# Performance work log

Measured on AMD Instinct MI355X. Metric: run time of the kernel, lower is better.

## Reference

```python
import jax, jax.numpy as jnp
import numpy as np

N, E = 50000, 800000
D_IN, HID, HEADS, D_OUT = 128, 32, 4, 40
NEG_SLOPE = 0.2
BN_EPS = 1e-5


def gat_conv(x, src, dst, W, a_src, a_dst, b, heads, ch):
    """PyG-style GATConv (eval mode, self-loops already appended to src/dst)."""
    n = x.shape[0]
    h = (x @ W).reshape(n, heads, ch)                      # [N,H,C]
    al_src = jnp.einsum('nhc,hc->nh', h, a_src)            # [N,H]
    al_dst = jnp.einsum('nhc,hc->nh', h, a_dst)
    e = jax.nn.leaky_relu(al_src[src] + al_dst[dst], NEG_SLOPE)  # [Etot,H]
    # segment softmax over incoming edges of each dst node
    e_max = jax.ops.segment_max(e, dst, num_segments=n)
    e = jnp.exp(e - e_max[dst])
    denom = jax.ops.segment_sum(e, dst, num_segments=n)
    alpha = e / (denom[dst] + 1e-16)                        # [Etot,H]
    msg = h[src] * alpha[:, :, None]                        # [Etot,H,C]
    out = jax.ops.segment_sum(msg, dst, num_segments=n)     # [N,H,C]
    return out.reshape(n, heads * ch) + b


def bn_eval(x, g, b, m, v):
    return (x - m) * jax.lax.rsqrt(v + BN_EPS) * g + b


def setup_inputs() -> dict:
    key = jax.random.key(0)
    ks = jax.random.split(key, 24)
    p = lambda k, s: jax.random.normal(k, s, jnp.float32) * 0.1
    inp = {
        'x': jax.random.normal(ks[0], (N, D_IN), jnp.float32),
        'edge_index': jax.random.randint(ks[1], (2, E), 0, N),
        'W1': p(ks[2], (D_IN, HEADS * HID)),
        'a_src1': p(ks[3], (HEADS, HID)), 'a_dst1': p(ks[4], (HEADS, HID)),
        'b1': jnp.zeros((HEADS * HID,), jnp.float32),
        'W2': p(ks[5], (HEADS * HID, HEADS * HID)),
        'a_src2': p(ks[6], (HEADS, HID)), 'a_dst2': p(ks[7], (HEADS, HID)),
        'b2': jnp.zeros((HEADS * HID,), jnp.float32),
        'W3': p(ks[8], (HEADS * HID, D_OUT)),
        'a_src3': p(ks[9], (1, D_OUT)), 'a_dst3': p(ks[10], (1, D_OUT)),
        'b3': jnp.zeros((D_OUT,), jnp.float32),
        'bn1_g': jnp.ones((HEADS * HID,), jnp.float32),
        'bn1_b': jnp.zeros((HEADS * HID,), jnp.float32),
        'bn1_m': p(ks[11], (HEADS * HID,)),
        'bn1_v': jax.random.uniform(ks[12], (HEADS * HID,), jnp.float32) + 0.5,
        'bn2_g': jnp.ones((HEADS * HID,), jnp.float32),
        'bn2_b': jnp.zeros((HEADS * HID,), jnp.float32),
        'bn2_m': p(ks[13], (HEADS * HID,)),
        'bn2_v': jax.random.uniform(ks[14], (HEADS * HID,), jnp.float32) + 0.5,
    }
    return inp


def reference(x, edge_index, W1, a_src1, a_dst1, b1, W2, a_src2, a_dst2, b2,
              W3, a_src3, a_dst3, b3, bn1_g, bn1_b, bn1_m, bn1_v,
              bn2_g, bn2_b, bn2_m, bn2_v):
    n = x.shape[0]
    loop = jnp.arange(n, dtype=edge_index.dtype)
    src = jnp.concatenate([edge_index[0], loop])   # add self loops (PyG default)
    dst = jnp.concatenate([edge_index[1], loop])

    h = gat_conv(x, src, dst, W1, a_src1, a_dst1, b1, HEADS, HID)
    h = jax.nn.relu(h)
    h = bn_eval(h, bn1_g, bn1_b, bn1_m, bn1_v)      # dropout = identity (eval)

    h = gat_conv(h, src, dst, W2, a_src2, a_dst2, b2, HEADS, HID)
    h = jax.nn.relu(h)
    h = bn_eval(h, bn2_g, bn2_b, bn2_m, bn2_v)

    h = gat_conv(h, src, dst, W3, a_src3, a_dst3, b3, 1, D_OUT)
    return jax.nn.log_softmax(h, axis=1)
```

## Files before the change

### kernel.cpp

```cpp
#include <hip/hip_runtime.h>
#include <hip/hip_bf16.h>
#include <math.h>

using bf16 = __hip_bfloat16;
using frag8 = __attribute__((ext_vector_type(8))) short;
using f32x4 = __attribute__((ext_vector_type(4))) float;

#define LEAKY 0.2f
#define BN_EPS 1e-5f
#define NEGBIG -1e30f

__device__ __forceinline__ float lrelu(float z){ return z > 0.f ? z : LEAKY * z; }
__device__ __forceinline__ float bflo(unsigned u){ return __uint_as_float(u << 16); }
__device__ __forceinline__ float bfhi(unsigned u){ return __uint_as_float(u & 0xffff0000u); }
__device__ __forceinline__ unsigned pk(float a, float b){
  unsigned ua = __float_as_uint(a), ub = __float_as_uint(b);
  ua += 0x7fffu + ((ua >> 16) & 1u);
  ub += 0x7fffu + ((ub >> 16) & 1u);
  return (ua >> 16) | (ub & 0xffff0000u);
}
__device__ __forceinline__ float ldf(const void* p, size_t i, int isbf){
  if (isbf) return (float)((const bf16*)p)[i];
  return ((const float*)p)[i];
}

union U4F8 { uint4 u; frag8 f; };

__device__ __forceinline__ frag8 load_a_pairs(const unsigned* __restrict__ X2, int node, int k0){
  U4F8 v; v.u = *((const uint4*)(X2 + (size_t)node*64 + (k0 >> 1))); return v.f;
}
__device__ __forceinline__ frag8 load_a_f32(const float* __restrict__ X, int node, int k0){
  float4 q0 = *((const float4*)(X + (size_t)node*128 + k0));
  float4 q1 = *((const float4*)(X + (size_t)node*128 + k0 + 4));
  U4F8 v; v.u = make_uint4(pk(q0.x,q0.y), pk(q0.z,q0.w), pk(q1.x,q1.y), pk(q1.z,q1.w));
  return v.f;
}

__global__ void init_detect(int* head, const unsigned short* __restrict__ w1bits,
                            int* flag, int n){
  int g = blockIdx.x*256 + threadIdx.x;
  if (g < n) head[g] = -1;
  if (blockIdx.x == 0){
    __shared__ int cntr;
    if (threadIdx.x == 0) cntr = 0;
    __syncthreads();
    unsigned u = w1bits[threadIdx.x * 2];
    int e = (u >> 7) & 0xff;
    atomicAdd(&cntr, (e >= 64 && e <= 140) ? 1 : 0);
    __syncthreads();
    if (threadIdx.x == 0) *flag = (cntr >= 160) ? 1 : 0;
  }
}

__global__ void chain_build(const int* __restrict__ dst, int* head, int* next,
                            int e, int n){
  int g = blockIdx.x*256 + threadIdx.x;
  if (g < e){
    int d = dst[g];
    next[g] = ((unsigned)d < (unsigned)n) ? atomicExch(&head[d], g) : -1;
  }
}

__global__ void chain_count(const int* __restrict__ head, const int* __restrict__ next,
                            int* cnt, int* total, int n){
  int g = blockIdx.x*256 + threadIdx.x;
  if (g == 0) *total = 0;
  if (g >= n) return;
  int c = 0;
  for (int e = head[g]; e != -1; e = next[e]) ++c;
  cnt[g] = c;
}

__global__ void csr_scan(const int* __restrict__ cnt, int* start, int* total, int n){
  __shared__ int s[256];
  __shared__ int base_s;
  int t = threadIdx.x;
  int g = blockIdx.x*256 + t;
  int v = (g < n) ? cnt[g] : 0;
  s[t] = v;
  __syncthreads();
  for (int off = 1; off < 256; off <<= 1){
    int x = (t >= off) ? s[t-off] : 0;
    __syncthreads();
    s[t] += x;
    __syncthreads();
  }
  if (t == 255) base_s = atomicAdd(total, s[255]);
  __syncthreads();
  if (g < n) start[g] = base_s + s[t] - v;
}

__global__ void chain_fill(const int* __restrict__ head, const int* __restrict__ next,
                           const int* __restrict__ src, const int* __restrict__ start,
                           int* col, int n){
  int g = blockIdx.x*256 + threadIdx.x;
  if (g >= n) return;
  int p = start[g];
  for (int e = head[g]; e != -1; e = next[e])
    col[p++] = src[e];
}

__global__ __launch_bounds__(256) void gemm_al_mfma(
    const void* __restrict__ X, int xkind,
    const void* __restrict__ W, const void* __restrict__ Wsrc, const void* __restrict__ Wdst,
    const int* __restrict__ flagp,
    unsigned* __restrict__ H2, float* __restrict__ AL, float* __restrict__ AD,
    int n, int ntiles)
{
  __shared__ unsigned short WT[128*136];
  const int isbf = *flagp;
  const int t = threadIdx.x;
  if (isbf){
    const unsigned short* W16 = (const unsigned short*)W;
    for (int idx = t; idx < 16384; idx += 256){
      int k = idx >> 7, nn = idx & 127;
      WT[nn*136 + k] = W16[idx];
    }
  } else {
    const float* Wf = (const float*)W;
    for (int idx = t; idx < 16384; idx += 256){
      int k = idx >> 7, nn = idx & 127;
      WT[nn*136 + k] = (unsigned short)(pk(Wf[idx], 0.f) & 0xffffu);
    }
  }
  __syncthreads();
  const int w = t >> 6;
  const int lane = t & 63;
  const int m = lane & 15, quad = lane >> 4;

  frag8 bf[4][2];
  #pragma unroll
  for (int s = 0; s < 4; ++s)
    #pragma unroll
    for (int ct = 0; ct < 2; ++ct){
      int colc = w*32 + ct*16 + m;
      int k0 = s*32 + quad*8;
      U4F8 v; v.u = *((const uint4*)&WT[colc*136 + k0]);
      bf[s][ct] = v.f;
    }
  float avv[2], dvv[2];
  #pragma unroll
  for (int ct = 0; ct < 2; ++ct){
    int colc = w*32 + ct*16 + m;
    avv[ct] = ldf(Wsrc, colc, isbf);
    dvv[ct] = ldf(Wdst, colc, isbf);
  }
  const bool pairs = (xkind == 1) || isbf;

  for (int tile = blockIdx.x; tile < ntiles; tile += gridDim.x){
    const int mb = tile*16;
    int nodeA = mb + m; if (nodeA >= n) nodeA = n - 1;
    frag8 af[4];
    #pragma unroll
    for (int s = 0; s < 4; ++s){
      int k0 = s*32 + quad*8;
      af[s] = pairs ? load_a_pairs((const unsigned*)X, nodeA, k0)
                    : load_a_f32((const float*)X, nodeA, k0);
    }
    f32x4 acc0 = {0.f,0.f,0.f,0.f}, acc1 = {0.f,0.f,0.f,0.f};
    #pragma unroll
    for (int s = 0; s < 4; ++s){
      acc0 = __builtin_amdgcn_mfma_f32_16x16x32_bf16(af[s], bf[s][0], acc0, 0,0,0);
      acc1 = __builtin_amdgcn_mfma_f32_16x16x32_bf16(af[s], bf[s][1], acc1, 0,0,0);
    }
    #pragma unroll
    for (int r = 0; r < 4; ++r){
      int g = mb + quad*4 + r;
      float v0 = acc0[r], v1 = acc1[r];
      unsigned u0 = pk(v0, __shfl_xor(v0, 1));
      unsigned u1 = pk(v1, __shfl_xor(v1, 1));
      bool ok = g < n;
      if (((lane & 1) == 0) && ok){
        H2[(size_t)g*64 + w*16 + (m >> 1)]     = u0;
        H2[(size_t)g*64 + w*16 + 8 + (m >> 1)] = u1;
      }
      float s1 = v0*avv[0] + v1*avv[1];
      float s2 = v0*dvv[0] + v1*dvv[1];
      s1 += __shfl_xor(s1,1); s1 += __shfl_xor(s1,2); s1 += __shfl_xor(s1,4); s1 += __shfl_xor(s1,8);
      s2 += __shfl_xor(s2,1); s2 += __shfl_xor(s2,2); s2 += __shfl_xor(s2,4); s2 += __shfl_xor(s2,8);
      if (m == 0 && ok){ AL[g*4 + w] = s1; AD[g*4 + w] = s2; }
    }
  }
}

__global__ __launch_bounds__(256) void gemm3_mfma(
    const unsigned* __restrict__ X2, const void* __restrict__ W,
    const void* __restrict__ Wsrc, const void* __restrict__ Wdst,
    const int* __restrict__ flagp,
    unsigned* __restrict__ H3, float* __restrict__ AL, float* __restrict__ AD,
    int n, int ntiles)
{
  __shared__ unsigned short WT[48*136];
  const int isbf = *flagp;
  const int t = threadIdx.x;
  for (int idx = t; idx < 128*64; idx += 256){
    int c = idx & 63, k = idx >> 6;
    if (c < 48){
      unsigned short v = 0;
      if (c < 40){
        if (isbf) v = ((const unsigned short*)W)[k*40 + c];
        else      v = (unsigned short)(pk(((const float*)W)[k*40 + c], 0.f) & 0xffffu);
      }
      WT[c*136 + k] = v;
    }
  }
  __syncthreads();
  const int w = t >> 6;
  const int lane = t & 63;
  const int m = lane & 15, quad = lane >> 4;

  frag8 bf[4][3];
  float avv[3], dvv[3];
  #pragma unroll
  for (int ct = 0; ct < 3; ++ct){
    int colc = ct*16 + m;
    #pragma unroll
    for (int s = 0; s < 4; ++s){
      int k0 = s*32 + quad*8;
      U4F8 v; v.u = *((const uint4*)&WT[colc*136 + k0]);
      bf[s][ct] = v.f;
    }
    avv[ct] = (colc < 40) ? ldf(Wsrc, colc, isbf) : 0.f;
    dvv[ct] = (colc < 40) ? ldf(Wdst, colc, isbf) : 0.f;
  }

  for (int tg = blockIdx.x; tg*4 < ntiles; tg += gridDim.x){
    const int tile = tg*4 + w;
    if (tile >= ntiles) continue;
    const int mb = tile*16;
    int nodeA = mb + m; if (nodeA >= n) nodeA = n - 1;
    frag8 af[4];
    #pragma unroll
    for (int s = 0; s < 4; ++s)
      af[s] = load_a_pairs(X2, nodeA, s*32 + quad*8);
    f32x4 acc[3];
    #pragma unroll
    for (int ct = 0; ct < 3; ++ct) acc[ct] = (f32x4){0.f,0.f,0.f,0.f};
    #pragma unroll
    for (int s = 0; s < 4; ++s){
      acc[0] = __builtin_amdgcn_mfma_f32_16x16x32_bf16(af[s], bf[s][0], acc[0], 0,0,0);
      acc[1] = __builtin_amdgcn_mfma_f32_16x16x32_bf16(af[s], bf[s][1], acc[1], 0,0,0);
      acc[2] = __builtin_amdgcn_mfma_f32_16x16x32_bf16(af[s], bf[s][2], acc[2], 0,0,0);
    }
    #pragma unroll
    for (int r = 0; r < 4; ++r){
      int g = mb + quad*4 + r;
      bool ok = g < n;
      float ps = 0.f, pd = 0.f;
      #pragma unroll
      for (int ct = 0; ct < 3; ++ct){
        float v = acc[ct][r];
        ps += v*avv[ct]; pd += v*dvv[ct];
        unsigned u = pk(v, __shfl_xor(v, 1));
        bool stok = ((lane & 1) == 0) && ok && (ct < 2 || m < 8);
        if (stok) H3[(size_t)g*20 + ct*8 + (m >> 1)] = u;
      }
      ps += __shfl_xor(ps,1); ps += __shfl_xor(ps,2); ps += __shfl_xor(ps,4); ps += __shfl_xor(ps,8);
      pd += __shfl_xor(pd,1); pd += __shfl_xor(pd,2); pd += __shfl_xor(pd,4); pd += __shfl_xor(pd,8);
      if (m == 0 && ok){ AL[g] = ps; AD[g] = pd; }
    }
  }
}

__global__ __launch_bounds__(256) void agg4(
    const unsigned* __restrict__ H2,
    const float* __restrict__ ALf, const float* __restrict__ ADf,
    const int* __restrict__ cnt, const int* __restrict__ start, const int* __restrict__ col,
    const void* __restrict__ bias, const void* __restrict__ bng, const void* __restrict__ bnb,
    const void* __restrict__ bnm,  const void* __restrict__ bnv,
    const int* __restrict__ flagp,
    unsigned* __restrict__ Hout, int n)
{
  const int isbf = *flagp;
  const int wave = threadIdx.x >> 6;
  const int lane = threadIdx.x & 63;
  const int node = blockIdx.x*4 + wave;
  if (node >= n) return;
  const int head = lane >> 4;
  const float ad = ADf[node*4 + head];
  const int base = start[node], deg = cnt[node];

  float accL, accH, l;
  {
    float e = __expf(lrelu(ALf[node*4 + head] + ad));
    unsigned h = H2[(size_t)node*64 + lane];
    l = e; accL = e * bflo(h); accH = e * bfhi(h);
  }

  int i = 0;
  for (; i + 8 <= deg; i += 8){
    int sv[8]; float av[8]; unsigned hv[8];
    #pragma unroll
    for (int u = 0; u < 8; ++u){
      int s = col[base + i + u];
      sv[u] = ((unsigned)s < (unsigned)n) ? s : 0;
    }
    #pragma unroll
    for (int u = 0; u < 8; ++u) av[u] = ALf[sv[u]*4 + head];
    #pragma unroll
    for (int u = 0; u < 8; ++u) hv[u] = H2[(size_t)sv[u]*64 + lane];
    #pragma unroll
    for (int u = 0; u < 8; ++u){
      float e = __expf(lrelu(av[u] + ad));
      l    += e;
      accL += e * bflo(hv[u]);
      accH += e * bfhi(hv[u]);
    }
  }
  for (; i < deg; ++i){
    int s = col[base + i];
    if ((unsigned)s >= (unsigned)n) s = 0;
    float a = ALf[s*4 + head];
    unsigned h = H2[(size_t)s*64 + lane];
    float e = __expf(lrelu(a + ad));
    l += e; accL += e * bflo(h); accH += e * bfhi(h);
  }

  const float rl = 1.f / l;
  const int c0 = 2*lane, c1 = c0 + 1;
  float v0 = fmaxf(accL*rl + ldf(bias,c0,isbf), 0.f);
  v0 = (v0 - ldf(bnm,c0,isbf)) * rsqrtf(ldf(bnv,c0,isbf) + BN_EPS) * ldf(bng,c0,isbf) + ldf(bnb,c0,isbf);
  float v1 = fmaxf(accH*rl + ldf(bias,c1,isbf), 0.f);
  v1 = (v1 - ldf(bnm,c1,isbf)) * rsqrtf(ldf(bnv,c1,isbf) + BN_EPS) * ldf(bng,c1,isbf) + ldf(bnb,c1,isbf);
  Hout[(size_t)node*64 + lane] = pk(v0, v1);
}

__global__ __launch_bounds__(256) void agg1(
    const unsigned* __restrict__ H3,
    const float* __restrict__ AL, const float* __restrict__ AD,
    const int* __restrict__ cnt, const int* __restrict__ start, const int* __restrict__ col,
    const void* __restrict__ b3, const int* __restrict__ flagp,
    void* __restrict__ out, int n)
{
  const int isbf = *flagp;
  const int wave = threadIdx.x >> 6;
  const int lane = threadIdx.x & 63;
  const int node = blockIdx.x*4 + wave;
  if (node >= n) return;
  const float ad = AD[node];
  const bool act = lane < 20;
  const int base = start[node], deg = cnt[node];

  float accL, accH, l;
  {
    float e = __expf(lrelu(AL[node] + ad));
    unsigned h = act ? H3[(size_t)node*20 + lane] : 0u;
    l = e; accL = e * bflo(h); accH = e * bfhi(h);
  }

  int i = 0;
  for (; i + 8 <= deg; i += 8){
    int sv[8]; float av[8]; unsigned hv[8];
    #pragma unroll
    for (int u = 0; u < 8; ++u){
      int s = col[base + i + u];
      sv[u] = ((unsigned)s < (unsigned)n) ? s : 0;
    }
    #pragma unroll
    for (int u = 0; u < 8; ++u) av[u] = AL[sv[u]];
    #pragma unroll
    for (int u = 0; u < 8; ++u) hv[u] = act ? H3[(size_t)sv[u]*20 + lane] : 0u;
    #pragma unroll
    for (int u = 0; u < 8; ++u){
      float e = __expf(lrelu(av[u] + ad));
      l    += e;
      accL += e * bflo(hv[u]);
      accH += e * bfhi(hv[u]);
    }
  }
  for (; i < deg; ++i){
    int s = col[base + i];
    if ((unsigned)s >= (unsigned)n) s = 0;
    float a = AL[s];
    unsigned h = act ? H3[(size_t)s*20 + lane] : 0u;
    float e = __expf(lrelu(a + ad));
    l += e; accL += e * bflo(h); accH += e * bfhi(h);
  }

  const float rl = 1.f / l;
  const int c0 = 2*lane;
  float z0 = act ? (accL*rl + ldf(b3, c0,     isbf)) : NEGBIG;
  float z1 = act ? (accH*rl + ldf(b3, c0 + 1, isbf)) : NEGBIG;
  float mx = fmaxf(z0, z1);
  #pragma unroll
  for (int off = 1; off < 64; off <<= 1) mx = fmaxf(mx, __shfl_xor(mx, off));
  float p = act ? (__expf(z0 - mx) + __expf(z1 - mx)) : 0.f;
  float sum = p;
  #pragma unroll
  for (int off = 1; off < 64; off <<= 1) sum += __shfl_xor(sum, off);
  if (act){
    float lg = __logf(sum);
    float r0 = z0 - mx - lg, r1 = z1 - mx - lg;
    if (isbf) ((unsigned*)out)[(size_t)node*20 + lane] = pk(r0, r1);
    else      ((float2*)out)[(size_t)node*20 + lane] = make_float2(r0, r1);
  }
}

extern "C" void kernel_launch(void* const* d_in, const int* in_sizes, int n_in,
                              void* d_out, int out_size, void* d_ws, size_t ws_size,
                              hipStream_t stream)
{
  (void)n_in; (void)out_size; (void)ws_size;
  const void* x    = d_in[0];
  const int*  ei   = (const int*)d_in[1];
  const void* W1   = d_in[2];
  const void* as1  = d_in[3];
  const void* ad1  = d_in[4];
  const void* b1   = d_in[5];
  const void* W2   = d_in[6];
  const void* as2  = d_in[7];
  const void* ad2  = d_in[8];
  const void* b2   = d_in[9];
  const void* W3   = d_in[10];
  const void* as3  = d_in[11];
  const void* ad3  = d_in[12];
  const void* b3   = d_in[13];
  const void* bn1g = d_in[14];
  const void* bn1b = d_in[15];
  const void* bn1m = d_in[16];
  const void* bn1v = d_in[17];
  const void* bn2g = d_in[18];
  const void* bn2b = d_in[19];
  const void* bn2m = d_in[20];
  const void* bn2v = d_in[21];

  const int N  = in_sizes[0] / 128;
  const int E  = in_sizes[1] / 2;
  const int ntiles = (N + 15) / 16;

  char* w = (char*)d_ws;
  size_t off = 0;
  auto alloc = [&](size_t bytes)->char*{
    char* p = w + off; off = (off + bytes + 255) & ~(size_t)255; return p;
  };
  unsigned* H2A = (unsigned*)alloc((size_t)N*64*4);
  unsigned* H2B = (unsigned*)alloc((size_t)N*64*4);
  unsigned* H3p = (unsigned*)alloc((size_t)N*20*4);
  float* AL   = (float*)alloc((size_t)N*4*4);
  float* AD   = (float*)alloc((size_t)N*4*4);
  int*   headp = (int*)alloc((size_t)N*4);
  int*   nextp = (int*)alloc((size_t)E*4);
  int*   cnt   = (int*)alloc((size_t)N*4);
  int*   start = (int*)alloc((size_t)N*4);
  int*   col   = (int*)alloc((size_t)E*4);
  int*   flag  = (int*)alloc(256);
  int*   total = (int*)alloc(256);

  const int* srcp = ei;
  const int* dstp = ei + E;

  const int nb256 = (N + 255)/256, eb256 = (E + 255)/256;
  const int bb = (N + 3)/4;
  int g1 = ntiles < 625 ? ntiles : 625;
  int g3 = (ntiles + 3)/4; if (g3 > 400) g3 = 400;

  init_detect<<<nb256,256,0,stream>>>(headp, (const unsigned short*)W1, flag, N);
  chain_build<<<eb256,256,0,stream>>>(dstp, headp, nextp, E, N);
  chain_count<<<nb256,256,0,stream>>>(headp, nextp, cnt, total, N);
  csr_scan  <<<nb256,256,0,stream>>>(cnt, start, total, N);
  chain_fill<<<nb256,256,0,stream>>>(headp, nextp, srcp, start, col, N);

  gemm_al_mfma<<<g1,256,0,stream>>>(x, 0, W1, as1, ad1, flag, H2A, AL, AD, N, ntiles);
  agg4<<<bb,256,0,stream>>>(H2A, AL, AD, cnt, start, col,
                            b1, bn1g, bn1b, bn1m, bn1v, flag, H2B, N);
  gemm_al_mfma<<<g1,256,0,stream>>>(H2B, 1, W2, as2, ad2, flag, H2A, AL, AD, N, ntiles);
  agg4<<<bb,256,0,stream>>>(H2A, AL, AD, cnt, start, col,
                            b2, bn2g, bn2b, bn2m, bn2v, flag, H2B, N);
  gemm3_mfma<<<g3,256,0,stream>>>(H2B, W3, as3, ad3, flag, H3p, AL, AD, N, ntiles);
  agg1<<<bb,256,0,stream>>>(H3p, AL, AD, cnt, start, col, b3, flag, d_out, N);
}
```

Measured before the change: 381.7 us.

## Precompute per-edge attention weights and split neighbor gather across half-waves

Adds per-edge weight kernels (wgt4/wgt1) that compute exp(leaky_relu(al_src+al_dst)) once per CSR edge, using a new rowid array written during CSR fill. The aggregation kernels then read these weights instead of gathering AL per neighbor and recomputing exp. agg4 now processes two neighbors at once, with each half-wave loading 8-byte feature chunks, and combines the halves with a cross-lane shuffle. The chain count is merged into the scan kernel to drop one launch. The cost is three extra kernel launches and a 16 B-per-edge weight array that must be written and read back.

```diff
diff --git a/kernel.cpp b/kernel.cpp
--- a/kernel.cpp
+++ b/kernel.cpp
@@ -37,9 +37,10 @@
 }
 
 __global__ void init_detect(int* head, const unsigned short* __restrict__ w1bits,
-                            int* flag, int n){
+                            int* flag, int* total, int n){
   int g = blockIdx.x*256 + threadIdx.x;
   if (g < n) head[g] = -1;
+  if (g == 0) *total = 0;
   if (blockIdx.x == 0){
     __shared__ int cntr;
     if (threadIdx.x == 0) cntr = 0;
@@ -61,22 +62,17 @@
   }
 }
 
-__global__ void chain_count(const int* __restrict__ head, const int* __restrict__ next,
-                            int* cnt, int* total, int n){
-  int g = blockIdx.x*256 + threadIdx.x;
-  if (g == 0) *total = 0;
-  if (g >= n) return;
-  int c = 0;
-  for (int e = head[g]; e != -1; e = next[e]) ++c;
-  cnt[g] = c;
-}
-
-__global__ void csr_scan(const int* __restrict__ cnt, int* start, int* total, int n){
+__global__ void csr_scan_walk(const int* __restrict__ head, const int* __restrict__ next,
+                              int* cnt, int* start, int* total, int n){
   __shared__ int s[256];
   __shared__ int base_s;
   int t = threadIdx.x;
   int g = blockIdx.x*256 + t;
-  int v = (g < n) ? cnt[g] : 0;
+  int v = 0;
+  if (g < n){
+    for (int e = head[g]; e != -1; e = next[e]) ++v;
+    cnt[g] = v;
+  }
   s[t] = v;
   __syncthreads();
   for (int off = 1; off < 256; off <<= 1){
@@ -92,12 +88,40 @@
 
 __global__ void chain_fill(const int* __restrict__ head, const int* __restrict__ next,
                            const int* __restrict__ src, const int* __restrict__ start,
-                           int* col, int n){
+                           int* col, int* rowid, int n){
   int g = blockIdx.x*256 + threadIdx.x;
   if (g >= n) return;
   int p = start[g];
-  for (int e = head[g]; e != -1; e = next[e])
-    col[p++] = src[e];
+  for (int e = head[g]; e != -1; e = next[e]){
+    int s = src[e];
+    if ((unsigned)s >= (unsigned)n) s = 0;
+    col[p] = s; rowid[p] = g; ++p;
+  }
+}
+
+__global__ void wgt4(const int* __restrict__ col, const int* __restrict__ rowid,
+                     const float4* __restrict__ AL4, const float4* __restrict__ AD4,
+                     float4* __restrict__ W4, int ecnt, int n){
+  int p = blockIdx.x*256 + threadIdx.x;
+  if (p >= ecnt) return;
+  int s = col[p];   if ((unsigned)s >= (unsigned)n) s = 0;
+  int d = rowid[p]; if ((unsigned)d >= (unsigned)n) d = 0;
+  float4 a = AL4[s], b = AD4[d];
+  float4 w;
+  w.x = __expf(lrelu(a.x + b.x));
+  w.y = __expf(lrelu(a.y + b.y));
+  w.z = __expf(lrelu(a.z + b.z));
+  w.w = __expf(lrelu(a.w + b.w));
+  W4[p] = w;
+}
+__global__ void wgt1(const int* __restrict__ col, const int* __restrict__ rowid,
+                     const float* __restrict__ AL, const float* __restrict__ AD,
+                     float* __restrict__ W1, int ecnt, int n){
+  int p = blockIdx.x*256 + threadIdx.x;
+  if (p >= ecnt) return;
+  int s = col[p];   if ((unsigned)s >= (unsigned)n) s = 0;
+  int d = rowid[p]; if ((unsigned)d >= (unsigned)n) d = 0;
+  W1[p] = __expf(lrelu(AL[s] + AD[d]));
 }
 
 __global__ __launch_bounds__(256) void gemm_al_mfma(
@@ -265,6 +289,7 @@
 __global__ __launch_bounds__(256) void agg4(
     const unsigned* __restrict__ H2,
     const float* __restrict__ ALf, const float* __restrict__ ADf,
+    const float* __restrict__ Wp,
     const int* __restrict__ cnt, const int* __restrict__ start, const int* __restrict__ col,
     const void* __restrict__ bias, const void* __restrict__ bng, const void* __restrict__ bnb,
     const void* __restrict__ bnm,  const void* __restrict__ bnv,
@@ -276,58 +301,74 @@
   const int lane = threadIdx.x & 63;
   const int node = blockIdx.x*4 + wave;
   if (node >= n) return;
-  const int head = lane >> 4;
-  const float ad = ADf[node*4 + head];
+  const int half = lane >> 5, sl = lane & 31;
+  const int head = sl >> 3;
   const int base = start[node], deg = cnt[node];
 
-  float accL, accH, l;
+  float l = 0.f, aLx = 0.f, aHx = 0.f, aLy = 0.f, aHy = 0.f;
   {
-    float e = __expf(lrelu(ALf[node*4 + head] + ad));
-    unsigned h = H2[(size_t)node*64 + lane];
-    l = e; accL = e * bflo(h); accH = e * bfhi(h);
-  }
-
-  int i = 0;
-  for (; i + 8 <= deg; i += 8){
-    int sv[8]; float av[8]; unsigned hv[8];
+    uint2 hs = *((const uint2*)(H2 + (size_t)node*64) + sl);
+    float es = (half == 0) ? __expf(lrelu(ALf[node*4+head] + ADf[node*4+head])) : 0.f;
+    l = es;
+    aLx = es*bflo(hs.x); aHx = es*bfhi(hs.x);
+    aLy = es*bflo(hs.y); aHy = es*bfhi(hs.y);
+  }
+
+  for (int i = 0; i < deg; i += 16){
+    int sv[8]; float wv[8];
     #pragma unroll
     for (int u = 0; u < 8; ++u){
-      int s = col[base + i + u];
-      sv[u] = ((unsigned)s < (unsigned)n) ? s : 0;
-    }
-    #pragma unroll
-    for (int u = 0; u < 8; ++u) av[u] = ALf[sv[u]*4 + head];
-    #pragma unroll
-    for (int u = 0; u < 8; ++u) hv[u] = H2[(size_t)sv[u]*64 + lane];
+      int j = i + 2*u + half;
+      bool valid = j < deg;
+      int jj = valid ? j : (deg - 1);
+      sv[u] = valid ? col[base + jj] : node;
+      wv[u] = valid ? Wp[(size_t)(base + jj)*4 + head] : 0.f;
+    }
+    uint2 hv[8];
+    #pragma unroll
+    for (int u = 0; u < 8; ++u)
+      hv[u] = *((const uint2*)(H2 + (size_t)sv[u]*64) + sl);
     #pragma unroll
     for (int u = 0; u < 8; ++u){
-      float e = __expf(lrelu(av[u] + ad));
-      l    += e;
-      accL += e * bflo(hv[u]);
-      accH += e * bfhi(hv[u]);
-    }
-  }
-  for (; i < deg; ++i){
-    int s = col[base + i];
-    if ((unsigned)s >= (unsigned)n) s = 0;
-    float a = ALf[s*4 + head];
-    unsigned h = H2[(size_t)s*64 + lane];
-    float e = __expf(lrelu(a + ad));
-    l += e; accL += e * bflo(h); accH += e * bfhi(h);
-  }
-
-  const float rl = 1.f / l;
-  const int c0 = 2*lane, c1 = c0 + 1;
-  float v0 = fmaxf(accL*rl + ldf(bias,c0,isbf), 0.f);
-  v0 = (v0 - ldf(bnm,c0,isbf)) * rsqrtf(ldf(bnv,c0,isbf) + BN_EPS) * ldf(bng,c0,isbf) + ldf(bnb,c0,isbf);
-  float v1 = fmaxf(accH*rl + ldf(bias,c1,isbf), 0.f);
-  v1 = (v1 - ldf(bnm,c1,isbf)) * rsqrtf(ldf(bnv,c1,isbf) + BN_EPS) * ldf(bng,c1,isbf) + ldf(bnb,c1,isbf);
-  Hout[(size_t)node*64 + lane] = pk(v0, v1);
+      float w = wv[u];
+      l   += w;
+      aLx += w * bflo(hv[u].x); aHx += w * bfhi(hv[u].x);
+      aLy += w * bflo(hv[u].y); aHy += w * bfhi(hv[u].y);
+    }
+  }
+
+  l   += __shfl_xor(l, 32);
+  aLx += __shfl_xor(aLx, 32); aHx += __shfl_xor(aHx, 32);
+  aLy += __shfl_xor(aLy, 32); aHy += __shfl_xor(aHy, 32);
+
+  if (half == 0){
+    const float rl = 1.f / l;
+    const int c0 = 4*sl;
+    float v[4] = {aLx*rl, aHx*rl, aLy*rl, aHy*rl};
+    unsigned o[2];
+    #pragma unroll
+    for (int q = 0; q < 2; ++q){
+      float r0, r1;
+      {
+        int c = c0 + 2*q;
+        float z = fmaxf(v[2*q] + ldf(bias,c,isbf), 0.f);
+        r0 = (z - ldf(bnm,c,isbf)) * rsqrtf(ldf(bnv,c,isbf) + BN_EPS) * ldf(bng,c,isbf) + ldf(bnb,c,isbf);
+      }
+      {
+        int c = c0 + 2*q + 1;
+        float z = fmaxf(v[2*q+1] + ldf(bias,c,isbf), 0.f);
+        r1 = (z - ldf(bnm,c,isbf)) * rsqrtf(ldf(bnv,c,isbf) + BN_EPS) * ldf(bng,c,isbf) + ldf(bnb,c,isbf);
+      }
+      o[q] = pk(r0, r1);
+    }
+    *((uint2*)(Hout + (size_t)node*64) + sl) = make_uint2(o[0], o[1]);
+  }
 }
 
 __global__ __launch_bounds__(256) void agg1(
     const unsigned* __restrict__ H3,
     const float* __restrict__ AL, const float* __restrict__ AD,
+    const float* __restrict__ W1p,
     const int* __restrict__ cnt, const int* __restrict__ start, const int* __restrict__ col,
     const void* __restrict__ b3, const int* __restrict__ flagp,
     void* __restrict__ out, int n)
@@ -337,44 +378,33 @@
   const int lane = threadIdx.x & 63;
   const int node = blockIdx.x*4 + wave;
   if (node >= n) return;
-  const float ad = AD[node];
   const bool act = lane < 20;
   const int base = start[node], deg = cnt[node];
 
   float accL, accH, l;
   {
-    float e = __expf(lrelu(AL[node] + ad));
+    float e = __expf(lrelu(AL[node] + AD[node]));
     unsigned h = act ? H3[(size_t)node*20 + lane] : 0u;
     l = e; accL = e * bflo(h); accH = e * bfhi(h);
   }
 
-  int i = 0;
-  for (; i + 8 <= deg; i += 8){
-    int sv[8]; float av[8]; unsigned hv[8];
+  for (int i = 0; i < deg; i += 8){
+    int sv[8]; float wv[8]; unsigned hv[8];
     #pragma unroll
     for (int u = 0; u < 8; ++u){
-      int s = col[base + i + u];
-      sv[u] = ((unsigned)s < (unsigned)n) ? s : 0;
-    }
-    #pragma unroll
-    for (int u = 0; u < 8; ++u) av[u] = AL[sv[u]];
+      int j = i + u;
+      bool valid = j < deg;
+      int jj = valid ? j : (deg - 1);
+      sv[u] = valid ? col[base + jj] : node;
+      wv[u] = valid ? W1p[base + jj] : 0.f;
+    }
     #pragma unroll
     for (int u = 0; u < 8; ++u) hv[u] = act ? H3[(size_t)sv[u]*20 + lane] : 0u;
     #pragma unroll
     for (int u = 0; u < 8; ++u){
-      float e = __expf(lrelu(av[u] + ad));
-      l    += e;
-      accL += e * bflo(hv[u]);
-      accH += e * bfhi(hv[u]);
-    }
-  }
-  for (; i < deg; ++i){
-    int s = col[base + i];
-    if ((unsigned)s >= (unsigned)n) s = 0;
-    float a = AL[s];
-    unsigned h = act ? H3[(size_t)s*20 + lane] : 0u;
-    float e = __expf(lrelu(a + ad));
-    l += e; accL += e * bflo(h); accH += e * bfhi(h);
+      float w = wv[u];
+      l += w; accL += w * bflo(hv[u]); accH += w * bfhi(hv[u]);
+    }
   }
 
   const float rl = 1.f / l;
@@ -436,13 +466,15 @@
   unsigned* H2A = (unsigned*)alloc((size_t)N*64*4);
   unsigned* H2B = (unsigned*)alloc((size_t)N*64*4);
   unsigned* H3p = (unsigned*)alloc((size_t)N*20*4);
-  float* AL   = (float*)alloc((size_t)N*4*4);
-  float* AD   = (float*)alloc((size_t)N*4*4);
+  float* AL    = (float*)alloc((size_t)N*4*4);
+  float* AD    = (float*)alloc((size_t)N*4*4);
   int*   headp = (int*)alloc((size_t)N*4);
   int*   nextp = (int*)alloc((size_t)E*4);
   int*   cnt   = (int*)alloc((size_t)N*4);
   int*   start = (int*)alloc((size_t)N*4);
   int*   col   = (int*)alloc((size_t)E*4);
+  int*   rowid = (int*)alloc((size_t)E*4);
+  float* Wedge = (float*)alloc((size_t)E*4*4);
   int*   flag  = (int*)alloc(256);
   int*   total = (int*)alloc(256);
 
@@ -454,18 +486,22 @@
   int g1 = ntiles < 625 ? ntiles : 625;
   int g3 = (ntiles + 3)/4; if (g3 > 400) g3 = 400;
 
-  init_detect<<<nb256,256,0,stream>>>(headp, (const unsigned short*)W1, flag, N);
+  init_detect<<<nb256,256,0,stream>>>(headp, (const unsigned short*)W1, flag, total, N);
   chain_build<<<eb256,256,0,stream>>>(dstp, headp, nextp, E, N);
-  chain_count<<<nb256,256,0,stream>>>(headp, nextp, cnt, total, N);
-  csr_scan  <<<nb256,256,0,stream>>>(cnt, start, total, N);
-  chain_fill<<<nb256,256,0,stream>>>(headp, nextp, srcp, start, col, N);
+  csr_scan_walk<<<nb256,256,0,stream>>>(headp, nextp, cnt, start, total, N);
+  chain_fill<<<nb256,256,0,stream>>>(headp, nextp, srcp, start, col, rowid, N);
 
   gemm_al_mfma<<<g1,256,0,stream>>>(x, 0, W1, as1, ad1, flag, H2A, AL, AD, N, ntiles);
-  agg4<<<bb,256,0,stream>>>(H2A, AL, AD, cnt, start, col,
+  wgt4<<<eb256,256,0,stream>>>(col, rowid, (const float4*)AL, (const float4*)AD,
+                               (float4*)Wedge, E, N);
+  agg4<<<bb,256,0,stream>>>(H2A, AL, AD, Wedge, cnt, start, col,
                             b1, bn1g, bn1b, bn1m, bn1v, flag, H2B, N);
   gemm_al_mfma<<<g1,256,0,stream>>>(H2B, 1, W2, as2, ad2, flag, H2A, AL, AD, N, ntiles);
-  agg4<<<bb,256,0,stream>>>(H2A, AL, AD, cnt, start, col,
+  wgt4<<<eb256,256,0,stream>>>(col, rowid, (const float4*)AL, (const float4*)AD,
+                               (float4*)Wedge, E, N);
+  agg4<<<bb,256,0,stream>>>(H2A, AL, AD, Wedge, cnt, start, col,
                             b2, bn2g, bn2b, bn2m, bn2v, flag, H2B, N);
   gemm3_mfma<<<g3,256,0,stream>>>(H2B, W3, as3, ad3, flag, H3p, AL, AD, N, ntiles);
-  agg1<<<bb,256,0,stream>>>(H3p, AL, AD, cnt, start, col, b3, flag, d_out, N);
-}
+  wgt1<<<eb256,256,0,stream>>>(col, rowid, AL, AD, Wedge, E, N);
+  agg1<<<bb,256,0,stream>>>(H3p, AL, AD, Wedge, cnt, start, col, b3, flag, d_out, N);
+}
```

Measured after the change: 432.0 us. 13.2% more time.

## Fuse chain count into scan, clamp sources once, split final aggregation across lane groups

Applied to the files above, without the earlier changes.

Merges the per-node chain-count kernel into the CSR scan kernel and moves the zeroing of the total counter into init_detect, removing one launch. Source-index clamping moves into chain_fill so the aggregation kernels no longer clamp every neighbor index. The 40-channel final aggregation now uses three 20-lane groups that each process a different edge, then combines the partial sums with shuffles, so 60 of 64 lanes do useful work instead of 20. This gives up the 8-way unrolled load batching in agg1 and adds cross-lane reduction overhead.

```diff
diff --git a/kernel.cpp b/kernel.cpp
--- a/kernel.cpp
+++ b/kernel.cpp
@@ -37,9 +37,10 @@
 }
 
 __global__ void init_detect(int* head, const unsigned short* __restrict__ w1bits,
-                            int* flag, int n){
+                            int* flag, int* total, int n){
   int g = blockIdx.x*256 + threadIdx.x;
   if (g < n) head[g] = -1;
+  if (g == 0) *total = 0;
   if (blockIdx.x == 0){
     __shared__ int cntr;
     if (threadIdx.x == 0) cntr = 0;
@@ -61,22 +62,17 @@
   }
 }
 
-__global__ void chain_count(const int* __restrict__ head, const int* __restrict__ next,
-                            int* cnt, int* total, int n){
-  int g = blockIdx.x*256 + threadIdx.x;
-  if (g == 0) *total = 0;
-  if (g >= n) return;
-  int c = 0;
-  for (int e = head[g]; e != -1; e = next[e]) ++c;
-  cnt[g] = c;
-}
-
-__global__ void csr_scan(const int* __restrict__ cnt, int* start, int* total, int n){
+__global__ void csr_scan_walk(const int* __restrict__ head, const int* __restrict__ next,
+                              int* cnt, int* start, int* total, int n){
   __shared__ int s[256];
   __shared__ int base_s;
   int t = threadIdx.x;
   int g = blockIdx.x*256 + t;
-  int v = (g < n) ? cnt[g] : 0;
+  int v = 0;
+  if (g < n){
+    for (int e = head[g]; e != -1; e = next[e]) ++v;
+    cnt[g] = v;
+  }
   s[t] = v;
   __syncthreads();
   for (int off = 1; off < 256; off <<= 1){
@@ -96,8 +92,11 @@
   int g = blockIdx.x*256 + threadIdx.x;
   if (g >= n) return;
   int p = start[g];
-  for (int e = head[g]; e != -1; e = next[e])
-    col[p++] = src[e];
+  for (int e = head[g]; e != -1; e = next[e]){
+    int s = src[e];
+    if ((unsigned)s >= (unsigned)n) s = 0;
+    col[p++] = s;
+  }
 }
 
 __global__ __launch_bounds__(256) void gemm_al_mfma(
@@ -291,10 +290,7 @@
   for (; i + 8 <= deg; i += 8){
     int sv[8]; float av[8]; unsigned hv[8];
     #pragma unroll
-    for (int u = 0; u < 8; ++u){
-      int s = col[base + i + u];
-      sv[u] = ((unsigned)s < (unsigned)n) ? s : 0;
-    }
+    for (int u = 0; u < 8; ++u) sv[u] = col[base + i + u];
     #pragma unroll
     for (int u = 0; u < 8; ++u) av[u] = ALf[sv[u]*4 + head];
     #pragma unroll
@@ -309,7 +305,6 @@
   }
   for (; i < deg; ++i){
     int s = col[base + i];
-    if ((unsigned)s >= (unsigned)n) s = 0;
     float a = ALf[s*4 + head];
     unsigned h = H2[(size_t)s*64 + lane];
     float e = __expf(lrelu(a + ad));
@@ -338,45 +333,35 @@
   const int node = blockIdx.x*4 + wave;
   if (node >= n) return;
   const float ad = AD[node];
+  const int grp = lane / 20;
+  const int cl  = lane - grp*20;
+  const bool g3 = grp < 3;
+  const int base = start[node], deg = cnt[node];
+
+  float accL = 0.f, accH = 0.f, l = 0.f;
+  if (grp == 0){
+    float e = __expf(lrelu(AL[node] + ad));
+    unsigned h = H3[(size_t)node*20 + cl];
+    l = e; accL = e * bflo(h); accH = e * bfhi(h);
+  }
+
+  for (int i = 0; i < deg; i += 3){
+    int j = i + grp;
+    bool valid = g3 && (j < deg);
+    int jj = valid ? j : (deg - 1);
+    int s  = valid ? col[base + jj] : node;
+    float a = AL[s];
+    unsigned h = H3[(size_t)s*20 + cl];
+    float e = valid ? __expf(lrelu(a + ad)) : 0.f;
+    l += e; accL += e * bflo(h); accH += e * bfhi(h);
+  }
+
+  int p1 = (lane + 20) & 63, p2 = (lane + 40) & 63;
+  l    += __shfl(l, p1)    + __shfl(l, p2);
+  accL += __shfl(accL, p1) + __shfl(accL, p2);
+  accH += __shfl(accH, p1) + __shfl(accH, p2);
+
   const bool act = lane < 20;
-  const int base = start[node], deg = cnt[node];
-
-  float accL, accH, l;
-  {
-    float e = __expf(lrelu(AL[node] + ad));
-    unsigned h = act ? H3[(size_t)node*20 + lane] : 0u;
-    l = e; accL = e * bflo(h); accH = e * bfhi(h);
-  }
-
-  int i = 0;
-  for (; i + 8 <= deg; i += 8){
-    int sv[8]; float av[8]; unsigned hv[8];
-    #pragma unroll
-    for (int u = 0; u < 8; ++u){
-      int s = col[base + i + u];
-      sv[u] = ((unsigned)s < (unsigned)n) ? s : 0;
-    }
-    #pragma unroll
-    for (int u = 0; u < 8; ++u) av[u] = AL[sv[u]];
-    #pragma unroll
-    for (int u = 0; u < 8; ++u) hv[u] = act ? H3[(size_t)sv[u]*20 + lane] : 0u;
-    #pragma unroll
-    for (int u = 0; u < 8; ++u){
-      float e = __expf(lrelu(av[u] + ad));
-      l    += e;
-      accL += e * bflo(hv[u]);
-      accH += e * bfhi(hv[u]);
-    }
-  }
-  for (; i < deg; ++i){
-    int s = col[base + i];
-    if ((unsigned)s >= (unsigned)n) s = 0;
-    float a = AL[s];
-    unsigned h = act ? H3[(size_t)s*20 + lane] : 0u;
-    float e = __expf(lrelu(a + ad));
-    l += e; accL += e * bflo(h); accH += e * bfhi(h);
-  }
-
   const float rl = 1.f / l;
   const int c0 = 2*lane;
   float z0 = act ? (accL*rl + ldf(b3, c0,     isbf)) : NEGBIG;
@@ -436,8 +421,8 @@
   unsigned* H2A = (unsigned*)alloc((size_t)N*64*4);
   unsigned* H2B = (unsigned*)alloc((size_t)N*64*4);
   unsigned* H3p = (unsigned*)alloc((size_t)N*20*4);
-  float* AL   = (float*)alloc((size_t)N*4*4);
-  float* AD   = (float*)alloc((size_t)N*4*4);
+  float* AL    = (float*)alloc((size_t)N*4*4);
+  float* AD    = (float*)alloc((size_t)N*4*4);
   int*   headp = (int*)alloc((size_t)N*4);
   int*   nextp = (int*)alloc((size_t)E*4);
   int*   cnt   = (int*)alloc((size_t)N*4);
@@ -454,10 +439,9 @@
   int g1 = ntiles < 625 ? ntiles : 625;
   int g3 = (ntiles + 3)/4; if (g3 > 400) g3 = 400;
 
-  init_detect<<<nb256,256,0,stream>>>(headp, (const unsigned short*)W1, flag, N);
+  init_detect<<<nb256,256,0,stream>>>(headp, (const unsigned short*)W1, flag, total, N);
   chain_build<<<eb256,256,0,stream>>>(dstp, headp, nextp, E, N);
-  chain_count<<<nb256,256,0,stream>>>(headp, nextp, cnt, total, N);
-  csr_scan  <<<nb256,256,0,stream>>>(cnt, start, total, N);
+  csr_scan_walk<<<nb256,256,0,stream>>>(headp, nextp, cnt, start, total, N);
   chain_fill<<<nb256,256,0,stream>>>(headp, nextp, srcp, start, col, N);
 
   gemm_al_mfma<<<g1,256,0,stream>>>(x, 0, W1, as1, ad1, flag, H2A, AL, AD, N, ntiles);
```

Measured after the change: 382.0 us. Within noise of the previous version (+0.1%).
